# Performance work log

Hardware: AMD Instinct MI355X
Metric: run time of the kernel (lower is better)

The kernel has to match this reference:

```python
import jax, jax.numpy as jnp
import numpy as np

B, N, N2 = 4, 4096, 4096
CIN, DIM, KNN, UP = 128, 64, 20, 2
HPOS, HATT = 64, 256
EPS = 1e-5


def _group(feat, idx):
    # feat: (B,C,M), idx: (B,N,K) -> (B,C,N,K) gather of neighbor features
    return jax.vmap(lambda f, i: f[:, i])(feat, idx)


def _conv1d(w, b, x):
    # 1x1 Conv1d: w (O,C), x (B,C,N)
    return jnp.einsum('oc,bcn->bon', w, x) + b[:, None]


def _bn(x, g, be, m, v):
    # eval-mode BatchNorm2d on (B,C,N,K)
    inv = g / jnp.sqrt(v + EPS)
    return x * inv[:, None, None] + (be - m * inv)[:, None, None]


def setup_inputs() -> dict:
    key = jax.random.key(0)
    ks = jax.random.split(key, 32)
    r = lambda i, s: jax.random.normal(ks[i], s, jnp.float32)
    u = lambda i, s: jax.random.uniform(ks[i], s, jnp.float32, 0.5, 1.5)
    return {
        'pos1': r(0, (B, 3, N)),
        'query': r(1, (B, CIN, N)),
        'pos2': r(2, (B, 3, N2)),
        'key_feat': r(3, (B, CIN, N2)),
        'wq': r(4, (DIM, CIN)) * 0.05, 'bq': r(5, (DIM,)) * 0.05,
        'wk': r(6, (DIM, CIN)) * 0.05, 'bk': r(7, (DIM,)) * 0.05,
        'wv': r(8, (DIM, CIN)) * 0.05, 'bv': r(9, (DIM,)) * 0.05,
        'pw1': r(10, (HPOS, 3)) * 0.2, 'pb1': r(11, (HPOS,)) * 0.05,
        'pg': u(12, (HPOS,)), 'pbt': r(13, (HPOS,)) * 0.05,
        'pm': r(14, (HPOS,)) * 0.05, 'pv': u(15, (HPOS,)),
        'pw2': r(16, (DIM, HPOS)) * 0.1, 'pb2': r(17, (DIM,)) * 0.05,
        'aw1': r(18, (HATT, DIM)) * 0.1, 'ab1': r(19, (HATT,)) * 0.05,
        'ag': u(20, (HATT,)), 'abt2': r(21, (HATT,)) * 0.05,
        'am': r(22, (HATT,)) * 0.05, 'av': u(23, (HATT,)),
        'awt': r(24, (HATT, DIM, UP)) * 0.05, 'abt': r(25, (DIM,)) * 0.05,
        'we': r(26, (CIN, DIM)) * 0.1, 'be': r(27, (CIN,)) * 0.05,
    }


def reference(pos1, query, pos2, key_feat, wq, bq, wk, bk, wv, bv,
              pw1, pb1, pg, pbt, pm, pv, pw2, pb2,
              aw1, ab1, ag, abt2, am, av, awt, abt, we, be):
    q = _conv1d(wq, bq, query)          # (B,DIM,N)
    k = _conv1d(wk, bk, key_feat)       # (B,DIM,N2)
    v = _conv1d(wv, bv, key_feat)       # (B,DIM,N2)
    # KNN of pos1 queries into pos2 support set
    p1 = pos1.transpose(0, 2, 1)        # (B,N,3)
    p2 = pos2.transpose(0, 2, 1)        # (B,N2,3)
    d = (jnp.sum(p1 * p1, -1)[:, :, None] + jnp.sum(p2 * p2, -1)[:, None, :]
         - 2.0 * jnp.einsum('bnd,bmd->bnm', p1, p2))
    _, idx = jax.lax.top_k(-d, KNN)     # (B,N,KNN)
    kg = _group(k, idx)                 # (B,DIM,N,K)
    qk_rel = q[:, :, :, None] - kg
    pos_rel = pos1[:, :, :, None] - _group(pos2, idx)   # (B,3,N,K)
    # pos_mlp: conv2d 3->HPOS, BN, ReLU, conv2d HPOS->DIM
    pe = jnp.einsum('oc,bcnk->bonk', pw1, pos_rel) + pb1[:, None, None]
    pe = jax.nn.relu(_bn(pe, pg, pbt, pm, pv))
    pe = jnp.einsum('oc,bcnk->bonk', pw2, pe) + pb2[:, None, None]  # (B,DIM,N,K)
    # attn_mlp: conv2d DIM->HATT, BN, ReLU, ConvTranspose2d HATT->DIM kernel (UP,1)
    h = qk_rel + pe
    a = jnp.einsum('oc,bcnk->bonk', aw1, h) + ab1[:, None, None]
    a = jax.nn.relu(_bn(a, ag, abt2, am, av))               # (B,HATT,N,K)
    att = jnp.einsum('bcnk,cor->bonrk', a, awt).reshape(B, DIM, N * UP, KNN)
    att = att + abt[:, None, None]
    att = jax.nn.softmax(att, axis=-1)
    vg = _group(v, idx) + pe            # (B,DIM,N,K)
    vu = jnp.repeat(vg, UP, axis=2)     # nearest upsample -> (B,DIM,N*UP,K)
    agg = jnp.sum(att * vu, axis=-1)    # (B,DIM,N*UP)
    y = _conv1d(we, be, agg)            # (B,CIN,N*UP)
    identity = jnp.repeat(query, UP, axis=2)  # residual (in==out -> Identity)
    return y + identity
```

## Files before the change

kernel.cpp:

```cpp
#include <hip/hip_runtime.h>
#include <hip/hip_bf16.h>

#define BATCH 4
#define NPTS  4096
#define NPTS2 4096
#define CIN   128
#define DIM   64
#define KNN   20
#define UPF   2
#define HPOS  64
#define HATT  256
#define MOUT  8192
#define EPSF  1e-5f
#define QPB   3
#define BPB   1366

#define FB_KNN   1024
#define FB_PKV   (FB_KNN + 256)
#define FB_PQ    (FB_PKV + 256)
#define FB_PACK  (FB_PQ + 128)

typedef _Float16 h16x8 __attribute__((ext_vector_type(8)));
typedef _Float16 h16x4 __attribute__((ext_vector_type(4)));
typedef _Float16 h16x2 __attribute__((ext_vector_type(2)));
typedef float    f32x4 __attribute__((ext_vector_type(4)));

__device__ inline float rdlane(float v, int src) {
  return __int_as_float(__builtin_amdgcn_readlane(__float_as_int(v), src));
}

__device__ __forceinline__ float distf(float qn, float m2x, float m2y, float m2z,
                                       float x, float y, float z) {
  float s = __fmaf_rn(x, x, qn);
  s = __fmaf_rn(y, y, s);
  s = __fmaf_rn(z, z, s);
  s = __fmaf_rn(m2x, x, s);
  s = __fmaf_rn(m2y, y, s);
  s = __fmaf_rn(m2z, z, s);
  return s;
}

__global__ __launch_bounds__(256) void front(
    const float* __restrict__ pos1, const float* __restrict__ pos2,
    int* __restrict__ idxout,
    const float* __restrict__ key_feat,
    const float* __restrict__ wk, const float* __restrict__ bk,
    const float* __restrict__ wv, const float* __restrict__ bv,
    float* __restrict__ k_t, float* __restrict__ v_t,
    const float* __restrict__ query,
    const float* __restrict__ wq, const float* __restrict__ bq,
    float* __restrict__ q_t,
    const float* __restrict__ aw1, const float* __restrict__ awt,
    const float* __restrict__ pw2,
    const float* __restrict__ ag,  const float* __restrict__ av,
    const float* __restrict__ abt2, const float* __restrict__ am,
    const float* __restrict__ abt,
    const float* __restrict__ pg,  const float* __restrict__ pv,
    const float* __restrict__ pbt, const float* __restrict__ pm,
    const float* __restrict__ ab1, const float* __restrict__ pb1,
    const float* __restrict__ pw1,
    _Float16* __restrict__ aw1h, _Float16* __restrict__ awtP,
    _Float16* __restrict__ pw2h, float* __restrict__ abtX,
    float* __restrict__ ab1f, float* __restrict__ pw1f,
    float* __restrict__ pb1f) {
  __shared__ union {
    struct { float X[CIN][64]; float O[64][65]; } pj;
    struct { int cnt[16]; float dbuf[16][64]; int jbuf[16][64]; } kn;
  } smU;
  const int bid = blockIdx.x;
  const int t   = threadIdx.x;

  if (bid < FB_KNN) {
    const int lane = t & 63;
    const int wv   = t >> 6;
    const int b    = bid >> 8;
    const int nb   = (bid & 255) * 16;
    const float* p2x = pos2 + (b * 3 + 0) * NPTS2;
    const float* p2y = pos2 + (b * 3 + 1) * NPTS2;
    const float* p2z = pos2 + (b * 3 + 2) * NPTS2;

    float qn[4], m2x[4], m2y[4], m2z[4];
#pragma unroll
    for (int qi = 0; qi < 4; ++qi) {
      int n = nb + wv * 4 + qi;
      float qx = pos1[(b * 3 + 0) * NPTS + n];
      float qy = pos1[(b * 3 + 1) * NPTS + n];
      float qz = pos1[(b * 3 + 2) * NPTS + n];
      qn[qi]  = qx * qx + qy * qy + qz * qz;
      m2x[qi] = -2.0f * qx; m2y[qi] = -2.0f * qy; m2z[qi] = -2.0f * qz;
    }

    float mymin[4] = {3.402823466e38f, 3.402823466e38f,
                      3.402823466e38f, 3.402823466e38f};
    f32x4 cx[4], cy[4], cz[4];
#pragma unroll 1
    for (int c = 0; c < 4; ++c) {
      int base = c * 1024 + lane * 4;
#pragma unroll
      for (int g = 0; g < 4; ++g) {
        cx[g] = *(const f32x4*)(p2x + base + g * 256);
        cy[g] = *(const f32x4*)(p2y + base + g * 256);
        cz[g] = *(const f32x4*)(p2z + base + g * 256);
      }
#pragma unroll
      for (int qi = 0; qi < 4; ++qi)
#pragma unroll
        for (int g = 0; g < 4; ++g)
#pragma unroll
          for (int e = 0; e < 4; ++e) {
            float d = distf(qn[qi], m2x[qi], m2y[qi], m2z[qi],
                            cx[g][e], cy[g][e], cz[g][e]);
            mymin[qi] = fminf(mymin[qi], d);
          }
    }

    float T0[4];
#pragma unroll
    for (int qi = 0; qi < 4; ++qi) {
      float v = mymin[qi];
#pragma unroll
      for (int k = 2; k <= 64; k <<= 1)
#pragma unroll
        for (int jj = k >> 1; jj >= 1; jj >>= 1) {
          float o = __shfl_xor(v, jj);
          bool up = ((lane & k) == 0);
          bool keepmin = (((lane & jj) == 0) == up);
          v = keepmin ? fminf(v, o) : fmaxf(v, o);
        }
      T0[qi] = rdlane(v, 19);
    }

    if (lane < 4) smU.kn.cnt[wv * 4 + lane] = 0;

#pragma unroll 1
    for (int c = 0; c < 4; ++c) {
      int base = c * 1024 + lane * 4;
#pragma unroll
      for (int g = 0; g < 4; ++g) {
        cx[g] = *(const f32x4*)(p2x + base + g * 256);
        cy[g] = *(const f32x4*)(p2y + base + g * 256);
        cz[g] = *(const f32x4*)(p2z + base + g * 256);
      }
#pragma unroll
      for (int qi = 0; qi < 4; ++qi) {
        const int qq = wv * 4 + qi;
#pragma unroll
        for (int g = 0; g < 4; ++g)
#pragma unroll
          for (int e = 0; e < 4; ++e) {
            float d = distf(qn[qi], m2x[qi], m2y[qi], m2z[qi],
                            cx[g][e], cy[g][e], cz[g][e]);
            if (d <= T0[qi]) {
              int slot = atomicAdd(&smU.kn.cnt[qq], 1);
              if (slot < 64) { smU.kn.dbuf[qq][slot] = d; smU.kn.jbuf[qq][slot] = base + g * 256 + e; }
            }
          }
      }
    }

#pragma unroll 1
    for (int qi = 0; qi < 4; ++qi) {
      const int qq = wv * 4 + qi;
      const int n  = nb + qq;
      const int cnt = smU.kn.cnt[qq];
      if (cnt <= 64) {
        float dk = (lane < cnt) ? smU.kn.dbuf[qq][lane] : 3.402823466e38f;
        int   jk = (lane < cnt) ? smU.kn.jbuf[qq][lane] : 0x7fffffff;
#pragma unroll
        for (int k = 2; k <= 64; k <<= 1) {
#pragma unroll
          for (int jj = k >> 1; jj >= 1; jj >>= 1) {
            float od = __shfl_xor(dk, jj);
            int   oj = __shfl_xor(jk, jj);
            bool mineSm = (dk < od) || (dk == od && jk < oj);
            bool up = ((lane & k) == 0);
            bool keepmin = (((lane & jj) == 0) == up);
            bool takeOther = (keepmin != mineSm);
            dk = takeOther ? od : dk;
            jk = takeOther ? oj : jk;
          }
        }
        if (lane < KNN) idxout[(b * NPTS + n) * KNN + lane] = jk;
      } else {
        float dl = 3.402823466e38f;
        int   il = 0;
        for (int j0 = 0; j0 < NPTS2; j0 += 64) {
          int j = j0 + lane;
          float d = distf(qn[qi], m2x[qi], m2y[qi], m2z[qi], p2x[j], p2y[j], p2z[j]);
          float T = rdlane(dl, 19);
          unsigned long long m = __ballot(d < T);
          while (m) {
            int src = __ffsll(m) - 1;
            m &= m - 1;
            float dd = rdlane(d, src);
            float T2 = rdlane(dl, 19);
            if (dd < T2) {
              int jj2 = j0 + src;
              float pd = __shfl_up(dl, 1);
              int   pi = __shfl_up(il, 1);
              if (dl > dd) {
                if (lane == 0 || pd <= dd) { dl = dd; il = jj2; }
                else                       { dl = pd; il = pi; }
              }
            }
          }
        }
        if (lane < KNN) idxout[(b * NPTS + n) * KNN + lane] = il;
      }
    }
  } else if (bid < FB_PKV) {
    const int vb = bid - FB_KNN;
    const int b  = vb >> 6;
    const int n0 = (vb & 63) * 64;
    for (int l = t; l < CIN * 64; l += 256) {
      int c = l >> 6, i = l & 63;
      smU.pj.X[c][i] = key_feat[(b * CIN + c) * NPTS2 + n0 + i];
    }
    __syncthreads();
    const int n_l = t & 63;
    const int w   = __builtin_amdgcn_readfirstlane(t >> 6);
    float acck[16], accv[16];
#pragma unroll
    for (int i = 0; i < 16; ++i) { acck[i] = bk[w * 16 + i]; accv[i] = bv[w * 16 + i]; }
    for (int c = 0; c < CIN; ++c) {
      float xv = smU.pj.X[c][n_l];
#pragma unroll
      for (int i = 0; i < 16; ++i) {
        acck[i] += wk[(w * 16 + i) * CIN + c] * xv;
        accv[i] += wv[(w * 16 + i) * CIN + c] * xv;
      }
    }
#pragma unroll
    for (int i = 0; i < 16; ++i) smU.pj.O[n_l][w * 16 + i] = acck[i];
    __syncthreads();
    for (int l = t; l < 64 * 64; l += 256)
      k_t[(b * NPTS2 + n0 + (l >> 6)) * DIM + (l & 63)] = smU.pj.O[l >> 6][l & 63];
    __syncthreads();
#pragma unroll
    for (int i = 0; i < 16; ++i) smU.pj.O[n_l][w * 16 + i] = accv[i];
    __syncthreads();
    for (int l = t; l < 64 * 64; l += 256)
      v_t[(b * NPTS2 + n0 + (l >> 6)) * DIM + (l & 63)] = smU.pj.O[l >> 6][l & 63];
  } else if (bid < FB_PQ) {
    const int vb = bid - FB_PKV;
    const int b  = vb >> 6;
    const int n0 = (vb & 63) * 64;
    for (int l = t; l < CIN * 64; l += 256) {
      int c = l >> 6, i = l & 63;
      smU.pj.X[c][i] = query[(b * CIN + c) * NPTS + n0 + i];
    }
    __syncthreads();
    const int n_l = t & 63;
    const int w   = __builtin_amdgcn_readfirstlane(t >> 6);
    float acc[16];
#pragma unroll
    for (int i = 0; i < 16; ++i) acc[i] = bq[w * 16 + i];
    for (int c = 0; c < CIN; ++c) {
      float xv = smU.pj.X[c][n_l];
#pragma unroll
      for (int i = 0; i < 16; ++i) acc[i] += wq[(w * 16 + i) * CIN + c] * xv;
    }
#pragma unroll
    for (int i = 0; i < 16; ++i) smU.pj.O[n_l][w * 16 + i] = acc[i];
    __syncthreads();
    for (int l = t; l < 64 * 64; l += 256)
      q_t[(b * NPTS + n0 + (l >> 6)) * DIM + (l & 63)] = smU.pj.O[l >> 6][l & 63];
  } else {
    int i = (bid - FB_PQ) * 256 + t;
    if (i < 16384) {
      int j = i >> 6;
      float inv = ag[j] / sqrtf(av[j] + EPSF);
      aw1h[i] = (_Float16)(aw1[i] * inv);
    }
    if (i < 32768) {
      int orr = i >> 8, j = i & 255;
      awtP[i] = (_Float16)awt[j * 128 + orr];
    }
    if (i < 4096) pw2h[i] = (_Float16)pw2[i];
    if (i < 256) {
      float inv = ag[i] / sqrtf(av[i] + EPSF);
      ab1f[i] = ab1[i] * inv + (abt2[i] - am[i] * inv);
    }
    if (i < 192) {
      int hc = i / 3;
      float inv = pg[hc] / sqrtf(pv[hc] + EPSF);
      pw1f[i] = pw1[i] * inv;
    }
    if (i < 128) abtX[i] = abt[i >> 1];
    if (i < 64) {
      float inv = pg[i] / sqrtf(pv[i] + EPSF);
      pb1f[i] = pb1[i] * inv + (pbt[i] - pm[i] * inv);
    }
  }
}

#define SM_R0    0
#define SM_R1    9216
#define SM_LGC   0
#define SM_VGB   18432

__global__ __launch_bounds__(256, 5) void attn_mfma(
    const float* __restrict__ q_t, const float* __restrict__ k_t,
    const float* __restrict__ v_t, const int* __restrict__ idx,
    const float* __restrict__ pos1, const float* __restrict__ pos2,
    const float* __restrict__ pw1f, const float* __restrict__ pb1f,
    const _Float16* __restrict__ pw2h, const float* __restrict__ pb2,
    const _Float16* __restrict__ aw1h, const float* __restrict__ ab1f,
    const _Float16* __restrict__ awtP, const float* __restrict__ abtX,
    float* __restrict__ agg) {
  __shared__ __align__(16) char smem[27136];
  const int b  = blockIdx.x / BPB;
  const int n0 = (blockIdx.x - b * BPB) * QPB;
  const int t  = threadIdx.x;
  const int lane = t & 63;
  const int w  = t >> 6;
  const int r  = lane & 15;
  const int q4 = lane >> 4;

  const int colB = t & 63, cgB = t >> 6;
  const int pB = colB / 20, kkB = colB - pB * 20;
  const bool okB = (pB < QPB) && (n0 + pB < NPTS);
  const int nqB = okB ? (n0 + pB) : 0;
  int jB = 0;
  if (okB) jB = idx[(b * NPTS + nqB) * KNN + kkB];

  f32x4 qk4[4], vv4[4];
  {
    const float* qrow = q_t + ((size_t)(b * NPTS  + nqB)) * DIM + cgB * 16;
    const float* krow = k_t + ((size_t)(b * NPTS2 + jB))  * DIM + cgB * 16;
    const float* vrow = v_t + ((size_t)(b * NPTS2 + jB))  * DIM + cgB * 16;
#pragma unroll
    for (int u = 0; u < 4; ++u) {
      f32x4 qv = *(const f32x4*)(qrow + u * 4);
      f32x4 kv = *(const f32x4*)(krow + u * 4);
      qk4[u] = qv - kv;
      vv4[u] = *(const f32x4*)(vrow + u * 4);
    }
  }

  {
    float p0 = 0.f, p1 = 0.f, p2 = 0.f;
    if (okB) {
      p0 = pos1[(b * 3 + 0) * NPTS + nqB] - pos2[(b * 3 + 0) * NPTS2 + jB];
      p1 = pos1[(b * 3 + 1) * NPTS + nqB] - pos2[(b * 3 + 1) * NPTS2 + jB];
      p2 = pos1[(b * 3 + 2) * NPTS + nqB] - pos2[(b * 3 + 2) * NPTS2 + jB];
    }
#pragma unroll
    for (int hf = 0; hf < 2; ++hf) {
      h16x8 pk;
#pragma unroll
      for (int ii = 0; ii < 8; ++ii) {
        int hc = cgB * 16 + hf * 8 + ii;
        float v0 = pb1f[hc] + pw1f[hc*3] * p0 + pw1f[hc*3+1] * p1 + pw1f[hc*3+2] * p2;
        v0 = fmaxf(v0, 0.f);
        if (!okB) v0 = 0.f;
        pk[ii] = (_Float16)v0;
      }
      *(h16x8*)(smem + SM_R0 + ((colB * 72 + cgB * 16 + hf * 8) * 2)) = pk;
    }
  }
  __syncthreads();

  {
    f32x4 acc[4];
#pragma unroll
    for (int nt = 0; nt < 4; ++nt) acc[nt] = (f32x4){0.f, 0.f, 0.f, 0.f};
#pragma unroll
    for (int ks = 0; ks < 2; ++ks) {
      h16x8 a0 = *(const h16x8*)&pw2h[(w * 16 + r) * 64 + ks * 32 + q4 * 8];
#pragma unroll
      for (int nt = 0; nt < 4; ++nt) {
        h16x8 bv = *(h16x8*)(smem + SM_R0 + ((nt * 16 + r) * 72 + ks * 32 + q4 * 8) * 2);
        acc[nt] = __builtin_amdgcn_mfma_f32_16x16x32_f16(a0, bv, acc[nt], 0, 0, 0);
      }
    }
    int o0 = w * 16 + q4 * 4;
    f32x4 pbv = *(const f32x4*)&pb2[o0];
#pragma unroll
    for (int nt = 0; nt < 4; ++nt) {
      f32x4 vv = acc[nt] + pbv;
      h16x4 pk = {(_Float16)vv[0], (_Float16)vv[1], (_Float16)vv[2], (_Float16)vv[3]};
      *(h16x4*)(smem + SM_R1 + ((nt * 16 + r) * 72 + o0) * 2) = pk;
    }
  }

  {
    h16x8 pe8[2];
#pragma unroll
    for (int hf = 0; hf < 2; ++hf)
      pe8[hf] = *(h16x8*)(smem + SM_R1 + (colB * 72 + cgB * 16 + hf * 8) * 2);
    h16x8 hp8[2];
#pragma unroll
    for (int u = 0; u < 4; ++u) {
      int hf = u >> 1, e0 = (u & 1) * 4;
      f32x4 pe = {(float)pe8[hf][e0],     (float)pe8[hf][e0 + 1],
                  (float)pe8[hf][e0 + 2], (float)pe8[hf][e0 + 3]};
      f32x4 hv = qk4[u] + pe;
      f32x4 gv = vv4[u] + pe;
      if (!okB) { hv = (f32x4){0.f,0.f,0.f,0.f}; gv = hv; }
      hp8[hf][e0]     = (_Float16)hv[0];
      hp8[hf][e0 + 1] = (_Float16)hv[1];
      hp8[hf][e0 + 2] = (_Float16)hv[2];
      hp8[hf][e0 + 3] = (_Float16)hv[3];
      h16x4 gp = {(_Float16)gv[0], (_Float16)gv[1], (_Float16)gv[2], (_Float16)gv[3]};
      *(h16x4*)(smem + SM_VGB + (colB * 68 + cgB * 16 + u * 4) * 2) = gp;
    }
#pragma unroll
    for (int hf = 0; hf < 2; ++hf)
      *(h16x8*)(smem + SM_R1 + (colB * 72 + cgB * 16 + hf * 8) * 2) = hp8[hf];
  }
  __syncthreads();

  f32x4 accD[2][4];
#pragma unroll
  for (int h = 0; h < 2; ++h)
#pragma unroll
    for (int nt = 0; nt < 4; ++nt) accD[h][nt] = (f32x4){0.f, 0.f, 0.f, 0.f};

#define C_QUARTER(quar)                                                        \
  {                                                                            \
    int mt = (quar) * 4 + w;                                                   \
    f32x4 acc[4];                                                              \
    _Pragma("unroll")                                                          \
    for (int nt = 0; nt < 4; ++nt) acc[nt] = (f32x4){0.f, 0.f, 0.f, 0.f};      \
    _Pragma("unroll")                                                          \
    for (int ks = 0; ks < 2; ++ks) {                                           \
      h16x8 af = *(const h16x8*)&aw1h[(mt * 16 + r) * 64 + ks * 32 + q4 * 8];  \
      h16x8 bsv[4];                                                            \
      _Pragma("unroll")                                                        \
      for (int nt = 0; nt < 4; ++nt)                                           \
        bsv[nt] = *(h16x8*)(smem + SM_R1 + ((nt * 16 + r) * 72 + ks * 32 + q4 * 8) * 2); \
      _Pragma("unroll")                                                        \
      for (int nt = 0; nt < 4; ++nt)                                           \
        acc[nt] = __builtin_amdgcn_mfma_f32_16x16x32_f16(af, bsv[nt], acc[nt], 0, 0, 0); \
    }                                                                          \
    int j0  = mt * 16 + q4 * 4;                                                \
    int jq0 = j0 - (quar) * 64;                                                \
    f32x4 b1 = *(const f32x4*)&ab1f[j0];                                       \
    _Pragma("unroll")                                                          \
    for (int nt = 0; nt < 4; ++nt) {                                           \
      int col = nt * 16 + r;                                                   \
      float v0 = fmaxf(acc[nt][0] + b1[0], 0.f);                               \
      float v1 = fmaxf(acc[nt][1] + b1[1], 0.f);                               \
      float v2 = fmaxf(acc[nt][2] + b1[2], 0.f);                               \
      float v3 = fmaxf(acc[nt][3] + b1[3], 0.f);                               \
      h16x4 pk = {(_Float16)v0, (_Float16)v1, (_Float16)v2, (_Float16)v3};     \
      *(h16x4*)(smem + SM_R0 + (col * 72 + jq0) * 2) = pk;                     \
    }                                                                          \
  }

#define D_QUARTER(quar)                                                        \
  {                                                                            \
    _Pragma("unroll")                                                          \
    for (int ks2 = 0; ks2 < 2; ++ks2) {                                        \
      h16x8 bsv[4];                                                            \
      _Pragma("unroll")                                                        \
      for (int nt = 0; nt < 4; ++nt)                                           \
        bsv[nt] = *(h16x8*)(smem + SM_R0 + ((nt * 16 + r) * 72 + ks2 * 32 + q4 * 8) * 2); \
      int ksg = (quar) * 2 + ks2;                                              \
      _Pragma("unroll")                                                        \
      for (int h = 0; h < 2; ++h) {                                            \
        int mt2 = w * 2 + h;                                                   \
        h16x8 af = *(const h16x8*)&awtP[(mt2 * 16 + r) * 256 + ksg * 32 + q4 * 8]; \
        _Pragma("unroll")                                                      \
        for (int nt = 0; nt < 4; ++nt)                                         \
          accD[h][nt] = __builtin_amdgcn_mfma_f32_16x16x32_f16(af, bsv[nt], accD[h][nt], 0, 0, 0); \
      }                                                                        \
    }                                                                          \
  }

  C_QUARTER(0)
  __syncthreads();
  D_QUARTER(0)
  __syncthreads();
  C_QUARTER(1)
  __syncthreads();
  D_QUARTER(1)
  __syncthreads();
  C_QUARTER(2)
  __syncthreads();
  D_QUARTER(2)
  __syncthreads();
  C_QUARTER(3)
  __syncthreads();
  D_QUARTER(3)
  __syncthreads();

  {
#pragma unroll
    for (int h = 0; h < 2; ++h) {
      int orr0 = (w * 2 + h) * 16 + q4 * 4;
      f32x4 ab = *(const f32x4*)&abtX[orr0];
#pragma unroll
      for (int nt = 0; nt < 4; ++nt) {
        int col = nt * 16 + r;
        if (col < QPB * KNN) {
          f32x4 vv = accD[h][nt] + ab;
          h16x4 pk = {(_Float16)vv[0], (_Float16)vv[1], (_Float16)vv[2], (_Float16)vv[3]};
          *(h16x4*)(smem + SM_LGC + (col * 136 + orr0) * 2) = pk;
        }
      }
    }
  }
  __syncthreads();

  if (t < 64 * QPB) {
    int li = t & 63, p = t >> 6;
    if (n0 + p < NPTS) {
      h16x2 Lp[KNN];
      float G[KNN];
#pragma unroll
      for (int kk = 0; kk < KNN; ++kk) {
        Lp[kk] = *(h16x2*)(smem + SM_LGC + ((p * 20 + kk) * 136 + li * 2) * 2);
        G[kk]  = (float)*(_Float16*)(smem + SM_VGB + ((p * 20 + kk) * 68 + li) * 2);
      }
#pragma unroll
      for (int half = 0; half < 2; ++half) {
        float mx = (float)Lp[0][half];
#pragma unroll
        for (int kk = 1; kk < KNN; ++kk) mx = fmaxf(mx, (float)Lp[kk][half]);
        float s = 0.f, a = 0.f;
#pragma unroll
        for (int kk = 0; kk < KNN; ++kk) {
          float e = __expf((float)Lp[kk][half] - mx);
          s += e;
          a += e * G[kk];
        }
        float rs = 1.0f / s;
        agg[(((size_t)(b * NPTS + n0 + p)) * UPF + half) * DIM + li] = a * rs;
      }
    }
  }
#undef C_QUARTER
#undef D_QUARTER
}

__global__ __launch_bounds__(256) void out_proj(const float* __restrict__ agg,
    const float* __restrict__ we, const float* __restrict__ be,
    const float* __restrict__ query, float* __restrict__ out) {
  __shared__ float A[64][65];
  const int b  = blockIdx.x >> 7;
  const int m0 = (blockIdx.x & 127) * 64;
  const int t  = threadIdx.x;
  for (int l = t; l < 64 * 64; l += 256) {
    int row = l >> 6, c = l & 63;
    A[row][c] = agg[(b * MOUT + m0 + row) * DIM + c];
  }
  __syncthreads();
  const int m_l = t & 63;
  const int w   = __builtin_amdgcn_readfirstlane(t >> 6);
  float acc[32];
#pragma unroll
  for (int i = 0; i < 32; ++i) acc[i] = 0.f;
  for (int c = 0; c < DIM; ++c) {
    float a = A[m_l][c];
#pragma unroll
    for (int i = 0; i < 32; ++i) acc[i] += we[(w * 32 + i) * DIM + c] * a;
  }
  const int m = m0 + m_l;
#pragma unroll
  for (int i = 0; i < 32; ++i) {
    int o = w * 32 + i;
    out[(b * CIN + o) * MOUT + m] = acc[i] + be[o] + query[(b * CIN + o) * NPTS + (m >> 1)];
  }
}

extern "C" void kernel_launch(void* const* d_in, const int* in_sizes, int n_in,
                              void* d_out, int out_size, void* d_ws, size_t ws_size,
                              hipStream_t stream) {
  (void)in_sizes; (void)n_in; (void)out_size; (void)ws_size;
  const float* pos1     = (const float*)d_in[0];
  const float* query    = (const float*)d_in[1];
  const float* pos2     = (const float*)d_in[2];
  const float* key_feat = (const float*)d_in[3];
  const float* wq  = (const float*)d_in[4];
  const float* bq  = (const float*)d_in[5];
  const float* wk  = (const float*)d_in[6];
  const float* bk  = (const float*)d_in[7];
  const float* wv  = (const float*)d_in[8];
  const float* bv  = (const float*)d_in[9];
  const float* pw1 = (const float*)d_in[10];
  const float* pb1 = (const float*)d_in[11];
  const float* pg  = (const float*)d_in[12];
  const float* pbt = (const float*)d_in[13];
  const float* pm  = (const float*)d_in[14];
  const float* pv  = (const float*)d_in[15];
  const float* pw2 = (const float*)d_in[16];
  const float* pb2 = (const float*)d_in[17];
  const float* aw1 = (const float*)d_in[18];
  const float* ab1 = (const float*)d_in[19];
  const float* ag  = (const float*)d_in[20];
  const float* abt2= (const float*)d_in[21];
  const float* am  = (const float*)d_in[22];
  const float* av  = (const float*)d_in[23];
  const float* awt = (const float*)d_in[24];
  const float* abt = (const float*)d_in[25];
  const float* we  = (const float*)d_in[26];
  const float* be  = (const float*)d_in[27];

  float* ws   = (float*)d_ws;
  float* q_t  = ws;
  float* k_t  = q_t + BATCH * NPTS * DIM;
  float* v_t  = k_t + BATCH * NPTS2 * DIM;
  float* aggb = v_t + BATCH * NPTS2 * DIM;
  int*   idxb = (int*)(aggb + BATCH * MOUT * DIM);
  _Float16* aw1h = (_Float16*)(idxb + BATCH * NPTS * KNN);
  _Float16* awtP = aw1h + HATT * DIM;
  _Float16* pw2h = awtP + 128 * HATT;
  float* abtX    = (float*)(pw2h + DIM * HPOS);
  float* ab1f    = abtX + 128;
  float* pw1f    = ab1f + HATT;
  float* pb1f    = pw1f + HPOS * 3;

  front<<<FB_PACK, 256, 0, stream>>>(
      pos1, pos2, idxb,
      key_feat, wk, bk, wv, bv, k_t, v_t,
      query, wq, bq, q_t,
      aw1, awt, pw2, ag, av, abt2, am, abt,
      pg, pv, pbt, pm, ab1, pb1, pw1,
      aw1h, awtP, pw2h, abtX, ab1f, pw1f, pb1f);
  attn_mfma<<<BATCH * BPB, 256, 0, stream>>>(q_t, k_t, v_t, idxb, pos1, pos2,
      pw1f, pb1f, pw2h, pb2, aw1h, ab1f, awtP, abtX, aggb);
  out_proj<<<BATCH * (MOUT / 64), 256, 0, stream>>>(aggb, we, be, query, (float*)d_out);
}
```

Measured before the change: 325.6 us.

## Process six query points per block with 128-column MFMA tiles

Doubles the number of query points each block handles from three to six, so each block's MFMA column tile grows from 64 to 128 (120 used). Each weight fragment loaded from global memory is reused across twice as many columns, and the padding waste per block shrinks. In exchange, shared memory doubles, launch bounds drop occupancy from 5 to 3 blocks, and accumulator register pressure roughly doubles, which risks spills.

```diff
diff --git a/kernel.cpp b/kernel.cpp
--- a/kernel.cpp
+++ b/kernel.cpp
@@ -12,8 +12,8 @@
 #define HATT  256
 #define MOUT  8192
 #define EPSF  1e-5f
-#define QPB   3
-#define BPB   1366
+#define QPB   6
+#define BPB   683
 
 #define FB_KNN   1024
 #define FB_PKV   (FB_KNN + 256)
@@ -295,11 +295,11 @@
 }
 
 #define SM_R0    0
-#define SM_R1    9216
+#define SM_R1    18432
 #define SM_LGC   0
-#define SM_VGB   18432
-
-__global__ __launch_bounds__(256, 5) void attn_mfma(
+#define SM_VGB   36864
+
+__global__ __launch_bounds__(256, 3) void attn_mfma(
     const float* __restrict__ q_t, const float* __restrict__ k_t,
     const float* __restrict__ v_t, const int* __restrict__ idx,
     const float* __restrict__ pos1, const float* __restrict__ pos2,
@@ -308,7 +308,7 @@
     const _Float16* __restrict__ aw1h, const float* __restrict__ ab1f,
     const _Float16* __restrict__ awtP, const float* __restrict__ abtX,
     float* __restrict__ agg) {
-  __shared__ __align__(16) char smem[27136];
+  __shared__ __align__(16) char smem[54272];
   const int b  = blockIdx.x / BPB;
   const int n0 = (blockIdx.x - b * BPB) * QPB;
   const int t  = threadIdx.x;
@@ -316,19 +316,24 @@
   const int w  = t >> 6;
   const int r  = lane & 15;
   const int q4 = lane >> 4;
-
-  const int colB = t & 63, cgB = t >> 6;
-  const int pB = colB / 20, kkB = colB - pB * 20;
-  const bool okB = (pB < QPB) && (n0 + pB < NPTS);
-  const int nqB = okB ? (n0 + pB) : 0;
-  int jB = 0;
-  if (okB) jB = idx[(b * NPTS + nqB) * KNN + kkB];
+  const int c0 = t & 63;
+  const int cgB = w;
+
+  int  jBh[2]; bool okh[2]; int nqh[2];
+#pragma unroll
+  for (int hl = 0; hl < 2; ++hl) {
+    int colB = c0 + hl * 64;
+    int pB = colB / 20;
+    okh[hl] = (pB < QPB) && (n0 + pB < NPTS);
+    nqh[hl] = okh[hl] ? (n0 + pB) : 0;
+    jBh[hl] = okh[hl] ? idx[(b * NPTS + nqh[hl]) * KNN + (colB - pB * 20)] : 0;
+  }
 
   f32x4 qk4[4], vv4[4];
   {
-    const float* qrow = q_t + ((size_t)(b * NPTS  + nqB)) * DIM + cgB * 16;
-    const float* krow = k_t + ((size_t)(b * NPTS2 + jB))  * DIM + cgB * 16;
-    const float* vrow = v_t + ((size_t)(b * NPTS2 + jB))  * DIM + cgB * 16;
+    const float* qrow = q_t + ((size_t)(b * NPTS  + nqh[0])) * DIM + cgB * 16;
+    const float* krow = k_t + ((size_t)(b * NPTS2 + jBh[0])) * DIM + cgB * 16;
+    const float* vrow = v_t + ((size_t)(b * NPTS2 + jBh[0])) * DIM + cgB * 16;
 #pragma unroll
     for (int u = 0; u < 4; ++u) {
       f32x4 qv = *(const f32x4*)(qrow + u * 4);
@@ -338,12 +343,14 @@
     }
   }
 
-  {
+#pragma unroll
+  for (int hl = 0; hl < 2; ++hl) {
+    int colB = c0 + hl * 64;
     float p0 = 0.f, p1 = 0.f, p2 = 0.f;
-    if (okB) {
-      p0 = pos1[(b * 3 + 0) * NPTS + nqB] - pos2[(b * 3 + 0) * NPTS2 + jB];
-      p1 = pos1[(b * 3 + 1) * NPTS + nqB] - pos2[(b * 3 + 1) * NPTS2 + jB];
-      p2 = pos1[(b * 3 + 2) * NPTS + nqB] - pos2[(b * 3 + 2) * NPTS2 + jB];
+    if (okh[hl]) {
+      p0 = pos1[(b * 3 + 0) * NPTS + nqh[hl]] - pos2[(b * 3 + 0) * NPTS2 + jBh[hl]];
+      p1 = pos1[(b * 3 + 1) * NPTS + nqh[hl]] - pos2[(b * 3 + 1) * NPTS2 + jBh[hl]];
+      p2 = pos1[(b * 3 + 2) * NPTS + nqh[hl]] - pos2[(b * 3 + 2) * NPTS2 + jBh[hl]];
     }
 #pragma unroll
     for (int hf = 0; hf < 2; ++hf) {
@@ -353,7 +360,7 @@
         int hc = cgB * 16 + hf * 8 + ii;
         float v0 = pb1f[hc] + pw1f[hc*3] * p0 + pw1f[hc*3+1] * p1 + pw1f[hc*3+2] * p2;
         v0 = fmaxf(v0, 0.f);
-        if (!okB) v0 = 0.f;
+        if (!okh[hl]) v0 = 0.f;
         pk[ii] = (_Float16)v0;
       }
       *(h16x8*)(smem + SM_R0 + ((colB * 72 + cgB * 16 + hf * 8) * 2)) = pk;
@@ -362,14 +369,14 @@
   __syncthreads();
 
   {
-    f32x4 acc[4];
-#pragma unroll
-    for (int nt = 0; nt < 4; ++nt) acc[nt] = (f32x4){0.f, 0.f, 0.f, 0.f};
+    f32x4 acc[8];
+#pragma unroll
+    for (int nt = 0; nt < 8; ++nt) acc[nt] = (f32x4){0.f, 0.f, 0.f, 0.f};
 #pragma unroll
     for (int ks = 0; ks < 2; ++ks) {
       h16x8 a0 = *(const h16x8*)&pw2h[(w * 16 + r) * 64 + ks * 32 + q4 * 8];
 #pragma unroll
-      for (int nt = 0; nt < 4; ++nt) {
+      for (int nt = 0; nt < 8; ++nt) {
         h16x8 bv = *(h16x8*)(smem + SM_R0 + ((nt * 16 + r) * 72 + ks * 32 + q4 * 8) * 2);
         acc[nt] = __builtin_amdgcn_mfma_f32_16x16x32_f16(a0, bv, acc[nt], 0, 0, 0);
       }
@@ -377,14 +384,28 @@
     int o0 = w * 16 + q4 * 4;
     f32x4 pbv = *(const f32x4*)&pb2[o0];
 #pragma unroll
-    for (int nt = 0; nt < 4; ++nt) {
+    for (int nt = 0; nt < 8; ++nt) {
       f32x4 vv = acc[nt] + pbv;
       h16x4 pk = {(_Float16)vv[0], (_Float16)vv[1], (_Float16)vv[2], (_Float16)vv[3]};
       *(h16x4*)(smem + SM_R1 + ((nt * 16 + r) * 72 + o0) * 2) = pk;
     }
   }
 
-  {
+#pragma unroll 1
+  for (int hl = 0; hl < 2; ++hl) {
+    int colB = c0 + hl * 64;
+    if (hl == 1) {
+      const float* qrow = q_t + ((size_t)(b * NPTS  + nqh[1])) * DIM + cgB * 16;
+      const float* krow = k_t + ((size_t)(b * NPTS2 + jBh[1])) * DIM + cgB * 16;
+      const float* vrow = v_t + ((size_t)(b * NPTS2 + jBh[1])) * DIM + cgB * 16;
+#pragma unroll
+      for (int u = 0; u < 4; ++u) {
+        f32x4 qv = *(const f32x4*)(qrow + u * 4);
+        f32x4 kv = *(const f32x4*)(krow + u * 4);
+        qk4[u] = qv - kv;
+        vv4[u] = *(const f32x4*)(vrow + u * 4);
+      }
+    }
     h16x8 pe8[2];
 #pragma unroll
     for (int hf = 0; hf < 2; ++hf)
@@ -397,7 +418,7 @@
                   (float)pe8[hf][e0 + 2], (float)pe8[hf][e0 + 3]};
       f32x4 hv = qk4[u] + pe;
       f32x4 gv = vv4[u] + pe;
-      if (!okB) { hv = (f32x4){0.f,0.f,0.f,0.f}; gv = hv; }
+      if (!okh[hl]) { hv = (f32x4){0.f,0.f,0.f,0.f}; gv = hv; }
       hp8[hf][e0]     = (_Float16)hv[0];
       hp8[hf][e0 + 1] = (_Float16)hv[1];
       hp8[hf][e0 + 2] = (_Float16)hv[2];
@@ -411,34 +432,34 @@
   }
   __syncthreads();
 
-  f32x4 accD[2][4];
+  f32x4 accD[2][8];
 #pragma unroll
   for (int h = 0; h < 2; ++h)
 #pragma unroll
-    for (int nt = 0; nt < 4; ++nt) accD[h][nt] = (f32x4){0.f, 0.f, 0.f, 0.f};
+    for (int nt = 0; nt < 8; ++nt) accD[h][nt] = (f32x4){0.f, 0.f, 0.f, 0.f};
 
 #define C_QUARTER(quar)                                                        \
   {                                                                            \
     int mt = (quar) * 4 + w;                                                   \
-    f32x4 acc[4];                                                              \
+    f32x4 acc[8];                                                              \
     _Pragma("unroll")                                                          \
-    for (int nt = 0; nt < 4; ++nt) acc[nt] = (f32x4){0.f, 0.f, 0.f, 0.f};      \
+    for (int nt = 0; nt < 8; ++nt) acc[nt] = (f32x4){0.f, 0.f, 0.f, 0.f};      \
     _Pragma("unroll")                                                          \
     for (int ks = 0; ks < 2; ++ks) {                                           \
       h16x8 af = *(const h16x8*)&aw1h[(mt * 16 + r) * 64 + ks * 32 + q4 * 8];  \
-      h16x8 bsv[4];                                                            \
+      h16x8 bsv[8];                                                            \
       _Pragma("unroll")                                                        \
-      for (int nt = 0; nt < 4; ++nt)                                           \
+      for (int nt = 0; nt < 8; ++nt)                                           \
         bsv[nt] = *(h16x8*)(smem + SM_R1 + ((nt * 16 + r) * 72 + ks * 32 + q4 * 8) * 2); \
       _Pragma("unroll")                                                        \
-      for (int nt = 0; nt < 4; ++nt)                                           \
+      for (int nt = 0; nt < 8; ++nt)                                           \
         acc[nt] = __builtin_amdgcn_mfma_f32_16x16x32_f16(af, bsv[nt], acc[nt], 0, 0, 0); \
     }                                                                          \
     int j0  = mt * 16 + q4 * 4;                                                \
     int jq0 = j0 - (quar) * 64;                                                \
     f32x4 b1 = *(const f32x4*)&ab1f[j0];                                       \
     _Pragma("unroll")                                                          \
-    for (int nt = 0; nt < 4; ++nt) {                                           \
+    for (int nt = 0; nt < 8; ++nt) {                                           \
       int col = nt * 16 + r;                                                   \
       float v0 = fmaxf(acc[nt][0] + b1[0], 0.f);                               \
       float v1 = fmaxf(acc[nt][1] + b1[1], 0.f);                               \
@@ -453,9 +474,9 @@
   {                                                                            \
     _Pragma("unroll")                                                          \
     for (int ks2 = 0; ks2 < 2; ++ks2) {                                        \
-      h16x8 bsv[4];                                                            \
+      h16x8 bsv[8];                                                            \
       _Pragma("unroll")                                                        \
-      for (int nt = 0; nt < 4; ++nt)                                           \
+      for (int nt = 0; nt < 8; ++nt)                                           \
         bsv[nt] = *(h16x8*)(smem + SM_R0 + ((nt * 16 + r) * 72 + ks2 * 32 + q4 * 8) * 2); \
       int ksg = (quar) * 2 + ks2;                                              \
       _Pragma("unroll")                                                        \
@@ -463,7 +484,7 @@
         int mt2 = w * 2 + h;                                                   \
         h16x8 af = *(const h16x8*)&awtP[(mt2 * 16 + r) * 256 + ksg * 32 + q4 * 8]; \
         _Pragma("unroll")                                                      \
-        for (int nt = 0; nt < 4; ++nt)                                         \
+        for (int nt = 0; nt < 8; ++nt)                                         \
           accD[h][nt] = __builtin_amdgcn_mfma_f32_16x16x32_f16(af, bsv[nt], accD[h][nt], 0, 0, 0); \
       }                                                                        \
     }                                                                          \
@@ -492,7 +513,7 @@
       int orr0 = (w * 2 + h) * 16 + q4 * 4;
       f32x4 ab = *(const f32x4*)&abtX[orr0];
 #pragma unroll
-      for (int nt = 0; nt < 4; ++nt) {
+      for (int nt = 0; nt < 8; ++nt) {
         int col = nt * 16 + r;
         if (col < QPB * KNN) {
           f32x4 vv = accD[h][nt] + ab;
@@ -504,9 +525,11 @@
   }
   __syncthreads();
 
-  if (t < 64 * QPB) {
-    int li = t & 63, p = t >> 6;
-    if (n0 + p < NPTS) {
+#pragma unroll 1
+  for (int it = 0; it < 2; ++it) {
+    int p  = (t >> 6) + it * 4;
+    int li = t & 63;
+    if (p < QPB && n0 + p < NPTS) {
       h16x2 Lp[KNN];
       float G[KNN];
 #pragma unroll
```

Result: faster. 314.4 us (-3.4%).
